# Kernel tuning notes

Measured on AMD Instinct MI355X. Metric: run time of the kernel, lower is better.

## Reference

```python
import jax, jax.numpy as jnp
import numpy as np
from jax import lax

B, T, N, D = 8, 64, 197, 768
HID = 4
K_FRAME, K_TOKEN = 8, 49
LAMBDA_COV, LAMBDA_SCORE = 1.0, 0.5
LN_EPS = 1e-5


def setup_inputs() -> dict:
    key = jax.random.key(0)
    k = jax.random.split(key, 5)
    x = jax.random.normal(k[0], (B, T, N, D), jnp.float32)
    mask = jax.random.uniform(k[1], (B, T, N), jnp.float32)
    ln_gamma = jnp.ones((D,), jnp.float32)
    ln_beta = jnp.zeros((D,), jnp.float32)
    W1 = jax.random.normal(k[2], (D, HID * D), jnp.float32) * 0.02
    b1 = jnp.zeros((HID * D,), jnp.float32)
    W2 = jax.random.normal(k[3], (HID * D, 1), jnp.float32) * 0.02
    b2 = jnp.zeros((1,), jnp.float32)
    return {"x": x, "mask": mask, "ln_gamma": ln_gamma, "ln_beta": ln_beta,
            "W1": W1, "b1": b1, "W2": W2, "b2": b2}


def _facility_location(frame_repr, score, valid, k):
    # cosine similarity between frames (F.normalize eps = 1e-12)
    fn = frame_repr / jnp.clip(jnp.linalg.norm(frame_repr, axis=-1, keepdims=True), 1e-12)
    sim = jnp.einsum('bid,bjd->bij', fn, fn)  # [B,T,T]
    Bb, Tt = score.shape

    def step(carry, _):
        best_cover, chosen = carry  # [B,T], [B,T] bool
        # coverage gain per candidate j: sum_i max(best[i], sim[i,j]) - best[i]
        cov_gain = jnp.maximum(best_cover[:, :, None], sim).sum(1) - best_cover.sum(1, keepdims=True)
        total = LAMBDA_COV * cov_gain + LAMBDA_SCORE * score
        total = jnp.where(valid & (~chosen), total, -jnp.inf)
        j = jnp.argmax(total, axis=1)  # [B]
        sim_j = jnp.take_along_axis(sim, j[:, None, None], axis=2)[..., 0]  # [B,T]
        best_cover = jnp.maximum(best_cover, sim_j)
        chosen = chosen.at[jnp.arange(Bb), j].set(True)
        return (best_cover, chosen), j

    init = (jnp.zeros((Bb, Tt), frame_repr.dtype), jnp.zeros((Bb, Tt), bool))
    (_, chosen), js = lax.scan(step, init, None, length=k)
    return js.T, chosen.astype(frame_repr.dtype)  # frame_idx [B,k], frame_mask [B,T]


def _kcenter(X, valid, k):
    # X [N,D], valid [N] bool; greedy k-center (farthest point sampling)
    d0 = jnp.where(valid, (X * X).sum(-1), -jnp.inf)
    first = jnp.argmax(d0)

    def dist_to(i):
        diff = X - X[i]
        return jnp.sqrt((diff * diff).sum(-1))

    min_dist = jnp.where(valid, dist_to(first), -1.0)

    def step(md, _):
        cand = jnp.argmax(md)
        md = jnp.where(valid, jnp.minimum(md, dist_to(cand)), -1.0)
        return md, cand

    _, rest = lax.scan(step, min_dist, None, length=k - 1)
    return jnp.concatenate([first[None], rest])


def _forward(x, mask, ln_gamma, ln_beta, W1, b1, W2, b2):
    # masked mean frame representation (use_cls=False path)
    denom = jnp.clip(mask.sum(2), 1e-6)                      # [B,T]
    frame_repr = (x * mask[..., None]).sum(2) / denom[..., None]  # [B,T,D]
    valid_frame = denom > 0

    # score head: LayerNorm -> Linear -> GELU(exact) -> Linear
    mu = frame_repr.mean(-1, keepdims=True)
    var = ((frame_repr - mu) ** 2).mean(-1, keepdims=True)
    h = (frame_repr - mu) / jnp.sqrt(var + LN_EPS) * ln_gamma + ln_beta
    h = jax.nn.gelu(h @ W1 + b1, approximate=False)
    score = (h @ W2 + b2)[..., 0]                            # [B,T]

    # selection is index-valued: no gradient flows through it (as in torch)
    frame_idx, frame_mask = _facility_location(
        lax.stop_gradient(frame_repr), lax.stop_gradient(score), valid_frame, K_FRAME)

    Xf = jnp.take_along_axis(x, frame_idx[:, :, None, None], axis=1)   # [B,K,N,D]
    mf = jnp.take_along_axis(mask, frame_idx[:, :, None], axis=1) > 0.5  # [B,K,N]

    token_idx = jax.vmap(jax.vmap(lambda Xs, vs: _kcenter(Xs, vs, K_TOKEN)))(
        lax.stop_gradient(Xf), mf)                           # [B,K,Kt]

    b_ar = jnp.arange(x.shape[0])
    token_mask = jnp.zeros(mask.shape, x.dtype).at[
        b_ar[:, None, None], frame_idx[:, :, None], token_idx].set(1.0)

    z = jnp.take_along_axis(Xf, token_idx[..., None], axis=2)  # [B,K,Kt,D]
    return z, frame_idx, token_idx, frame_mask, token_mask


def reference(x, mask, ln_gamma, ln_beta, W1, b1, W2, b2):
    return _forward(x, mask, ln_gamma, ln_beta, W1, b1, W2, b2)
```

## Files before the change

### kernel.cpp

```cpp
#include <hip/hip_runtime.h>
#include <math.h>

#define B_ 8
#define T_ 64
#define N_ 197
#define D_ 768
#define HIDD_ 3072
#define KF_ 8
#define KT_ 49
#define GSTRIDE 200

#define Z_SZ    (B_*KF_*KT_*D_)
#define FI_OFF  (Z_SZ)
#define TI_OFF  (FI_OFF + B_*KF_)
#define FM_OFF  (TI_OFF + B_*KF_*KT_)
#define TM_OFF  (FM_OFF + B_*T_)
#define TM_SZ   (B_*T_*N_)

#define WS_SCOREP  0
#define WS_FN64    98304
#define WS_H32     (WS_FN64 + 3145728)
#define WS_VALID   (WS_H32 + 1572864)
#define WS_FIDX    (WS_VALID + 2048)
#define WS_SIM     (WS_FIDX + 256)
#define WS_G       (WS_SIM + 262144)

__global__ __launch_bounds__(256) void kA(const float* __restrict__ x,
                                          const float* __restrict__ mask,
                                          const float* __restrict__ gamma,
                                          const float* __restrict__ beta,
                                          double* __restrict__ fn64,
                                          float* __restrict__ h32,
                                          int* __restrict__ validw) {
  const int row = blockIdx.x;
  const int tid = threadIdx.x;
  __shared__ float  ms[N_];
  __shared__ double red[256];
  __shared__ double sh_denom, sh_mu, sh_sd, sh_nrm;
  const float* xr = x + (size_t)row * (N_ * D_);

  if (tid < N_) ms[tid] = mask[(size_t)row * N_ + tid];
  __syncthreads();

  red[tid] = (tid < N_) ? (double)ms[tid] : 0.0;
  __syncthreads();
  for (int s = 128; s > 0; s >>= 1) { if (tid < s) red[tid] += red[tid + s]; __syncthreads(); }
  if (tid == 0) { double d = red[0]; sh_denom = (d > 1e-6) ? d : 1e-6; }
  __syncthreads();
  const double dn = sh_denom;

  double a0 = 0.0, a1 = 0.0, a2 = 0.0, a3 = 0.0;
  if (tid < 192) {
    const float* px = xr + tid * 4;
#pragma unroll 4
    for (int n = 0; n < N_; n++) {
      const double mv = (double)ms[n];
      const float4 v = *(const float4*)(px + (size_t)n * D_);
      a0 += (double)v.x * mv;
      a1 += (double)v.y * mv;
      a2 += (double)v.z * mv;
      a3 += (double)v.w * mv;
    }
  }
  const double f0 = a0 / dn, f1 = a1 / dn, f2 = a2 / dn, f3 = a3 / dn;

  red[tid] = (tid < 192) ? (f0 + f1 + f2 + f3) : 0.0; __syncthreads();
  for (int s = 128; s > 0; s >>= 1) { if (tid < s) red[tid] += red[tid + s]; __syncthreads(); }
  if (tid == 0) sh_mu = red[0] / (double)D_;
  __syncthreads();
  const double mu = sh_mu;

  red[tid] = (tid < 192) ? (f0 * f0 + f1 * f1 + f2 * f2 + f3 * f3) : 0.0; __syncthreads();
  for (int s = 128; s > 0; s >>= 1) { if (tid < s) red[tid] += red[tid + s]; __syncthreads(); }
  if (tid == 0) { double nr = sqrt(red[0]); sh_nrm = (nr > 1e-12) ? nr : 1e-12; }
  __syncthreads();

  red[tid] = (tid < 192) ? ((f0 - mu) * (f0 - mu) + (f1 - mu) * (f1 - mu) +
                            (f2 - mu) * (f2 - mu) + (f3 - mu) * (f3 - mu)) : 0.0;
  __syncthreads();
  for (int s = 128; s > 0; s >>= 1) { if (tid < s) red[tid] += red[tid + s]; __syncthreads(); }
  if (tid == 0) sh_sd = sqrt(red[0] / (double)D_ + 1e-5);
  __syncthreads();
  const double sd = sh_sd, nrm = sh_nrm;

  if (tid < 192) {
    const size_t base = (size_t)row * D_;
    const float4 g  = ((const float4*)gamma)[tid];
    const float4 be = ((const float4*)beta)[tid];
    float4 hv;
    hv.x = (float)((f0 - mu) / sd * (double)g.x + (double)be.x);
    hv.y = (float)((f1 - mu) / sd * (double)g.y + (double)be.y);
    hv.z = (float)((f2 - mu) / sd * (double)g.z + (double)be.z);
    hv.w = (float)((f3 - mu) / sd * (double)g.w + (double)be.w);
    *(float4*)(h32 + base + tid * 4) = hv;
    double2* fp = (double2*)(fn64 + base + tid * 4);
    fp[0] = make_double2(f0 / nrm, f1 / nrm);
    fp[1] = make_double2(f2 / nrm, f3 / nrm);
  }
  if (tid == 0) validw[row] = 1;
}

__global__ __launch_bounds__(256) void kB(const float* __restrict__ h32,
                                          const float* __restrict__ W1,
                                          const float* __restrict__ b1,
                                          const float* __restrict__ W2,
                                          double* __restrict__ scorep) {
  const int n0 = blockIdx.x * 128;
  const int m0 = blockIdx.y * 32;
  const int tid = threadIdx.x;
  const int tx = tid & 31;
  const int ty = tid >> 5;
  __shared__ float As[64 * 36];
  __shared__ float Bs[64 * 128];
  float acc[4][4];
#pragma unroll
  for (int r = 0; r < 4; r++)
#pragma unroll
    for (int c = 0; c < 4; c++) acc[r][c] = 0.0f;

  for (int kc = 0; kc < 12; kc++) {
    const int k0 = kc * 64;
#pragma unroll
    for (int it = 0; it < 8; it++) {
      int idx = tid + (it << 8);
      int k = idx & 63, m = idx >> 6;
      As[k * 36 + m] = h32[(size_t)(m0 + m) * D_ + k0 + k];
    }
#pragma unroll
    for (int it = 0; it < 8; it++) {
      int idx = tid + (it << 8);
      int k = idx >> 5, n4 = idx & 31;
      const float4 v = *(const float4*)(W1 + (size_t)(k0 + k) * HIDD_ + n0 + (n4 << 2));
      *(float4*)(Bs + k * 128 + (n4 << 2)) = v;
    }
    __syncthreads();
#pragma unroll 16
    for (int kk = 0; kk < 64; kk++) {
      float4 av = *(const float4*)(As + kk * 36 + ty * 4);
      float4 bv = *(const float4*)(Bs + kk * 128 + tx * 4);
      const float a[4] = {av.x, av.y, av.z, av.w};
      const float bb[4] = {bv.x, bv.y, bv.z, bv.w};
#pragma unroll
      for (int r = 0; r < 4; r++)
#pragma unroll
        for (int c = 0; c < 4; c++) acc[r][c] += a[r] * bb[c];
    }
    __syncthreads();
  }

  double part[4] = {0.0, 0.0, 0.0, 0.0};
#pragma unroll
  for (int r = 0; r < 4; r++) {
#pragma unroll
    for (int c = 0; c < 4; c++) {
      const int gn = n0 + tx * 4 + c;
      const double v = (double)(acc[r][c] + b1[gn]);
      const double g = 0.5 * v * (1.0 + erf(v * 0.7071067811865475244));
      part[r] += g * (double)W2[gn];
    }
  }
#pragma unroll
  for (int r = 0; r < 4; r++) {
    double s = part[r];
#pragma unroll
    for (int off = 16; off > 0; off >>= 1) s += __shfl_down(s, off, 32);
    if (tx == 0) scorep[(size_t)(m0 + ty * 4 + r) * 24 + blockIdx.x] = s;
  }
}

__global__ __launch_bounds__(256) void kS(const double* __restrict__ fn64,
                                          double* __restrict__ simG) {
  const int b    = blockIdx.x >> 2;
  const int tile = blockIdx.x & 3;
  const int tid = threadIdx.x;
  const int ty = tid >> 4;
  const int tx = tid & 15;
  __shared__ double As[64 * 17];
  __shared__ double Bs[64 * 66];
  double acc[4] = {0.0, 0.0, 0.0, 0.0};

  for (int kc = 0; kc < 12; kc++) {
#pragma unroll
    for (int it = 0; it < 4; it++) {
      const int idx = (it << 8) + tid;
      const int row = idx >> 6, kk = idx & 63;
      As[kk * 17 + row] = fn64[((size_t)(b * T_ + tile * 16 + row)) * D_ + kc * 64 + kk];
    }
#pragma unroll
    for (int it = 0; it < 16; it++) {
      const int idx = (it << 8) + tid;
      const int row = idx >> 6, kk = idx & 63;
      Bs[kk * 66 + row] = fn64[((size_t)(b * T_ + row)) * D_ + kc * 64 + kk];
    }
    __syncthreads();
#pragma unroll 8
    for (int kk = 0; kk < 64; kk++) {
      const double a = As[kk * 17 + ty];
      const double* bp = Bs + kk * 66 + tx * 4;
      acc[0] += a * bp[0];
      acc[1] += a * bp[1];
      acc[2] += a * bp[2];
      acc[3] += a * bp[3];
    }
    __syncthreads();
  }
  double* o = simG + ((size_t)b * 64 + tile * 16 + ty) * 64 + tx * 4;
  o[0] = acc[0]; o[1] = acc[1]; o[2] = acc[2]; o[3] = acc[3];
}

__global__ __launch_bounds__(256) void kD(const double* __restrict__ simG,
                                          const double* __restrict__ scorep,
                                          const int* __restrict__ validw,
                                          const float* __restrict__ b2,
                                          int* __restrict__ fidxw,
                                          float* __restrict__ out_fidx,
                                          float* __restrict__ out_fmask) {
  const int b = blockIdx.x;
  const int tid = threadIdx.x;
  __shared__ double sim[64 * 64];
  __shared__ double scoreS[64];
  __shared__ double bc[64];
  __shared__ int chosenS[64];
  __shared__ int validS[64];

  const double2* sp = (const double2*)(simG + (size_t)b * 4096);
#pragma unroll
  for (int it = 0; it < 8; it++) {
    const int idx = (it << 8) + tid;
    ((double2*)sim)[idx] = sp[idx];
  }
  if (tid < 64) {
    double s = 0.0;
    const double* pp = scorep + (size_t)(b * T_ + tid) * 24;
    for (int q = 0; q < 24; q++) s += pp[q];
    scoreS[tid]  = s + (double)b2[0];
    validS[tid]  = validw[b * T_ + tid];
    bc[tid]      = 0.0;
    chosenS[tid] = 0;
  }
  __syncthreads();

  for (int step = 0; step < KF_; step++) {
    if (tid < 64) {
      double g = 0.0;
      for (int ii = 0; ii < 64; ii++) g += fmax(bc[ii], sim[ii * 64 + tid]);
      double bs = bc[tid];
#pragma unroll
      for (int off = 32; off > 0; off >>= 1) bs += __shfl_down(bs, off, 64);
      bs = __shfl(bs, 0, 64);
      double tot = g - bs + 0.5 * scoreS[tid];
      if (!validS[tid] || chosenS[tid]) tot = -INFINITY;
      double bv = tot; int bi = tid;
#pragma unroll
      for (int off = 32; off > 0; off >>= 1) {
        double ov = __shfl_down(bv, off, 64);
        int    oi = __shfl_down(bi, off, 64);
        if (ov > bv || (ov == bv && oi < bi)) { bv = ov; bi = oi; }
      }
      bi = __shfl(bi, 0, 64);
      bc[tid] = fmax(bc[tid], sim[tid * 64 + bi]);
      if (tid == bi) chosenS[tid] = 1;
      if (tid == 0) {
        fidxw[b * KF_ + step] = bi;
        out_fidx[b * KF_ + step] = (float)bi;
      }
    }
    __syncthreads();
  }
  if (tid < 64) out_fmask[b * T_ + tid] = chosenS[tid] ? 1.0f : 0.0f;
}

__global__ __launch_bounds__(256) void kG(const float* __restrict__ x,
                                          const int* __restrict__ fidxw,
                                          double* __restrict__ G) {
  static const int TIa[10] = {0,0,0,0,1,1,1,2,2,3};
  static const int TJa[10] = {0,1,2,3,1,2,3,2,3,3};
  const int p  = blockIdx.x / 10;
  const int t  = blockIdx.x - p * 10;
  const int ti = TIa[t], tj = TJa[t];
  const int b  = p >> 3;
  const int fi = fidxw[p];
  const float* X = x + ((size_t)(b * T_ + fi)) * (N_ * D_);
  double* Gp = G + (size_t)p * (GSTRIDE * GSTRIDE);

  __shared__ float As[32 * 68];
  __shared__ float Bs[32 * 68];
  const int tid = threadIdx.x;
  const int tx = tid & 15;
  const int ty = tid >> 4;
  double acc[4][4];
#pragma unroll
  for (int r = 0; r < 4; r++)
#pragma unroll
    for (int c = 0; c < 4; c++) acc[r][c] = 0.0;

  for (int kc = 0; kc < 24; kc++) {
#pragma unroll
    for (int it = 0; it < 2; it++) {
      const int idx = (it << 8) + tid;
      const int row = idx >> 3;
      const int kg  = idx & 7;
      const int gra = ti * 64 + row, grb = tj * 64 + row;
      const int ra = (gra < N_) ? gra : (N_ - 1);
      const int rb = (grb < N_) ? grb : (N_ - 1);
      const float4 va = *(const float4*)(X + (size_t)ra * D_ + kc * 32 + kg * 4);
      const float4 vb = *(const float4*)(X + (size_t)rb * D_ + kc * 32 + kg * 4);
      As[(kg * 4 + 0) * 68 + row] = va.x;
      As[(kg * 4 + 1) * 68 + row] = va.y;
      As[(kg * 4 + 2) * 68 + row] = va.z;
      As[(kg * 4 + 3) * 68 + row] = va.w;
      Bs[(kg * 4 + 0) * 68 + row] = vb.x;
      Bs[(kg * 4 + 1) * 68 + row] = vb.y;
      Bs[(kg * 4 + 2) * 68 + row] = vb.z;
      Bs[(kg * 4 + 3) * 68 + row] = vb.w;
    }
    __syncthreads();
#pragma unroll 8
    for (int kk = 0; kk < 32; kk++) {
      const float4 av = *(const float4*)(As + kk * 68 + ty * 4);
      const float4 bv = *(const float4*)(Bs + kk * 68 + tx * 4);
      const double a[4]  = {(double)av.x, (double)av.y, (double)av.z, (double)av.w};
      const double bb[4] = {(double)bv.x, (double)bv.y, (double)bv.z, (double)bv.w};
#pragma unroll
      for (int r = 0; r < 4; r++)
#pragma unroll
        for (int c = 0; c < 4; c++) acc[r][c] += a[r] * bb[c];
    }
    __syncthreads();
  }

#pragma unroll
  for (int r = 0; r < 4; r++) {
    const int gi = ti * 64 + ty * 4 + r;
#pragma unroll
    for (int c = 0; c < 4; c++) {
      const int gj = tj * 64 + tx * 4 + c;
      if (gi < N_ && gj < N_) {
        Gp[(size_t)gi * GSTRIDE + gj] = acc[r][c];
        if (ti != tj) Gp[(size_t)gj * GSTRIDE + gi] = acc[r][c];
      }
    }
  }
}

__global__ __launch_bounds__(256) void kE2(const double* __restrict__ G,
                                           const float* __restrict__ mask,
                                           const int* __restrict__ fidxw,
                                           const float* __restrict__ x,
                                           float* __restrict__ out) {
  const int p = blockIdx.x;
  const int b = p >> 3;
  const int fi = fidxw[p];
  const double* Gp = G + (size_t)p * (GSTRIDE * GSTRIDE);
  const float* mrow = mask + (size_t)(b * T_ + fi) * N_;
  const float* X = x + ((size_t)(b * T_ + fi)) * (N_ * D_);
  const int tid = threadIdx.x;
  const bool live = tid < N_;

  __shared__ double gds[N_];
  __shared__ double bvS[4];
  __shared__ int biS[4];
  __shared__ int candS;
  __shared__ int toksS[KT_];

  const int valid = (live && mrow[tid] > 0.5f) ? 1 : 0;
  const double gd = live ? Gp[(size_t)tid * GSTRIDE + tid] : 0.0;
  if (live) gds[tid] = gd;
  __syncthreads();

  auto argmax = [&](double v) -> int {
    double bv = v; int bi = tid;
#pragma unroll
    for (int off = 32; off > 0; off >>= 1) {
      const double ov = __shfl_down(bv, off, 64);
      const int    oi = __shfl_down(bi, off, 64);
      if (ov > bv || (ov == bv && oi < bi)) { bv = ov; bi = oi; }
    }
    const int w = tid >> 6;
    if ((tid & 63) == 0) { bvS[w] = bv; biS[w] = bi; }
    __syncthreads();
    if (tid == 0) {
      double B0 = bvS[0]; int best = biS[0];
      for (int q = 1; q < 4; q++)
        if (bvS[q] > B0) { B0 = bvS[q]; best = biS[q]; }
      candS = best;
    }
    __syncthreads();
    return candS;
  };

  int cand = argmax((live && valid) ? gd : -INFINITY);
  if (tid == 0) toksS[0] = cand;

  double md = -INFINITY;
  for (int k = 1; k < KT_; k++) {
    const double gdc = gds[cand];
    const double g = live ? Gp[(size_t)cand * GSTRIDE + tid] : 0.0;
    const double dist = sqrt(fmax(gd + gdc - 2.0 * g, 0.0));
    if (live) md = valid ? ((k == 1) ? dist : fmin(md, dist)) : -1.0;
    cand = argmax(md);
    if (tid == 0) toksS[k] = cand;
  }
  __syncthreads();

  if (tid < KT_) {
    const int tok = toksS[tid];
    out[TI_OFF + p * KT_ + tid] = (float)tok;
    out[TM_OFF + (size_t)(b * T_ + fi) * N_ + tok] = 1.0f;
  }
  if (tid < 192) {
    for (int r = 0; r < KT_; r++) {
      const float4 v = *(const float4*)(X + (size_t)toksS[r] * D_ + tid * 4);
      *(float4*)(out + ((size_t)(p * KT_ + r)) * D_ + tid * 4) = v;
    }
  }
}

extern "C" void kernel_launch(void* const* d_in, const int* in_sizes, int n_in,
                              void* d_out, int out_size, void* d_ws, size_t ws_size,
                              hipStream_t stream) {
  (void)in_sizes; (void)n_in; (void)ws_size; (void)out_size;
  const float* x     = (const float*)d_in[0];
  const float* mask  = (const float*)d_in[1];
  const float* gamma = (const float*)d_in[2];
  const float* beta  = (const float*)d_in[3];
  const float* W1    = (const float*)d_in[4];
  const float* b1    = (const float*)d_in[5];
  const float* W2    = (const float*)d_in[6];
  const float* b2    = (const float*)d_in[7];
  float* out = (float*)d_out;
  char* ws = (char*)d_ws;

  double* scorep = (double*)(ws + WS_SCOREP);
  double* fn64   = (double*)(ws + WS_FN64);
  float*  h32    = (float*)(ws + WS_H32);
  int*    validw = (int*)(ws + WS_VALID);
  int*    fidxw  = (int*)(ws + WS_FIDX);
  double* simG   = (double*)(ws + WS_SIM);
  double* G      = (double*)(ws + WS_G);

  hipMemsetAsync(out + TM_OFF, 0, (size_t)TM_SZ * sizeof(float), stream);

  kA<<<B_ * T_, 256, 0, stream>>>(x, mask, gamma, beta, fn64, h32, validw);
  kS<<<B_ * 4, 256, 0, stream>>>(fn64, simG);
  kB<<<dim3(HIDD_ / 128, (B_ * T_) / 32), 256, 0, stream>>>(h32, W1, b1, W2, scorep);
  kD<<<B_, 256, 0, stream>>>(simG, scorep, validw, b2, fidxw, out + FI_OFF, out + FM_OFF);
  kG<<<B_ * KF_ * 10, 256, 0, stream>>>(x, fidxw, G);
  kE2<<<B_ * KF_, 256, 0, stream>>>(G, mask, fidxw, x, out);
}
```

Measured before the change: 762.3 us.

## Merge sim and score kernels; run greedy selections in single wavefront

Combines the double-precision similarity GEMM and the MLP scoring GEMM into one launch, with block ranges split by blockIdx, which removes a kernel launch and lets the two independent workloads share the GPU. The facility-location and k-center greedy loops are rewritten to run inside one 64-lane wavefront, keeping state in registers and using xor-shuffle argmax reductions instead of shared memory plus block-wide barriers. The validity check in facility location is dropped because every frame is marked valid. The trade-off is fewer active lanes in k-center, with each lane now handling four points.

```diff
diff --git a/kernel.cpp b/kernel.cpp
--- a/kernel.cpp
+++ b/kernel.cpp
@@ -100,117 +100,120 @@
   if (tid == 0) validw[row] = 1;
 }
 
-__global__ __launch_bounds__(256) void kB(const float* __restrict__ h32,
-                                          const float* __restrict__ W1,
-                                          const float* __restrict__ b1,
-                                          const float* __restrict__ W2,
-                                          double* __restrict__ scorep) {
-  const int n0 = blockIdx.x * 128;
-  const int m0 = blockIdx.y * 32;
+__global__ __launch_bounds__(256) void kSB(const double* __restrict__ fn64,
+                                           double* __restrict__ simG,
+                                           const float* __restrict__ h32,
+                                           const float* __restrict__ W1,
+                                           const float* __restrict__ b1,
+                                           const float* __restrict__ W2,
+                                           double* __restrict__ scorep) {
+  __shared__ char smem[42496] __attribute__((aligned(16)));
   const int tid = threadIdx.x;
-  const int tx = tid & 31;
-  const int ty = tid >> 5;
-  __shared__ float As[64 * 36];
-  __shared__ float Bs[64 * 128];
-  float acc[4][4];
-#pragma unroll
-  for (int r = 0; r < 4; r++)
-#pragma unroll
-    for (int c = 0; c < 4; c++) acc[r][c] = 0.0f;
-
-  for (int kc = 0; kc < 12; kc++) {
-    const int k0 = kc * 64;
-#pragma unroll
-    for (int it = 0; it < 8; it++) {
-      int idx = tid + (it << 8);
-      int k = idx & 63, m = idx >> 6;
-      As[k * 36 + m] = h32[(size_t)(m0 + m) * D_ + k0 + k];
-    }
-#pragma unroll
-    for (int it = 0; it < 8; it++) {
-      int idx = tid + (it << 8);
-      int k = idx >> 5, n4 = idx & 31;
-      const float4 v = *(const float4*)(W1 + (size_t)(k0 + k) * HIDD_ + n0 + (n4 << 2));
-      *(float4*)(Bs + k * 128 + (n4 << 2)) = v;
-    }
-    __syncthreads();
+
+  if (blockIdx.x < 32) {
+    const int b    = blockIdx.x >> 2;
+    const int tile = blockIdx.x & 3;
+    const int ty = tid >> 4;
+    const int tx = tid & 15;
+    double* As = (double*)smem;
+    double* Bs = (double*)(smem + 8704);
+    double acc[4] = {0.0, 0.0, 0.0, 0.0};
+
+    for (int kc = 0; kc < 12; kc++) {
+#pragma unroll
+      for (int it = 0; it < 4; it++) {
+        const int idx = (it << 8) + tid;
+        const int row = idx >> 6, kk = idx & 63;
+        As[kk * 17 + row] = fn64[((size_t)(b * T_ + tile * 16 + row)) * D_ + kc * 64 + kk];
+      }
+#pragma unroll
+      for (int it = 0; it < 16; it++) {
+        const int idx = (it << 8) + tid;
+        const int row = idx >> 6, kk = idx & 63;
+        Bs[kk * 66 + row] = fn64[((size_t)(b * T_ + row)) * D_ + kc * 64 + kk];
+      }
+      __syncthreads();
+#pragma unroll 8
+      for (int kk = 0; kk < 64; kk++) {
+        const double a = As[kk * 17 + ty];
+        const double* bp = Bs + kk * 66 + tx * 4;
+        acc[0] += a * bp[0];
+        acc[1] += a * bp[1];
+        acc[2] += a * bp[2];
+        acc[3] += a * bp[3];
+      }
+      __syncthreads();
+    }
+    double* o = simG + ((size_t)b * 64 + tile * 16 + ty) * 64 + tx * 4;
+    o[0] = acc[0]; o[1] = acc[1]; o[2] = acc[2]; o[3] = acc[3];
+  } else {
+    const int bid2 = blockIdx.x - 32;
+    const int nb = bid2 % 24;
+    const int n0 = nb * 128;
+    const int m0 = (bid2 / 24) * 32;
+    const int tx = tid & 31;
+    const int ty = tid >> 5;
+    float* As = (float*)smem;
+    float* Bs = (float*)(smem + 9216);
+    float acc[4][4];
+#pragma unroll
+    for (int r = 0; r < 4; r++)
+#pragma unroll
+      for (int c = 0; c < 4; c++) acc[r][c] = 0.0f;
+
+    for (int kc = 0; kc < 12; kc++) {
+      const int k0 = kc * 64;
+#pragma unroll
+      for (int it = 0; it < 8; it++) {
+        int idx = tid + (it << 8);
+        int k = idx & 63, m = idx >> 6;
+        As[k * 36 + m] = h32[(size_t)(m0 + m) * D_ + k0 + k];
+      }
+#pragma unroll
+      for (int it = 0; it < 8; it++) {
+        int idx = tid + (it << 8);
+        int k = idx >> 5, n4 = idx & 31;
+        const float4 v = *(const float4*)(W1 + (size_t)(k0 + k) * HIDD_ + n0 + (n4 << 2));
+        *(float4*)(Bs + k * 128 + (n4 << 2)) = v;
+      }
+      __syncthreads();
 #pragma unroll 16
-    for (int kk = 0; kk < 64; kk++) {
-      float4 av = *(const float4*)(As + kk * 36 + ty * 4);
-      float4 bv = *(const float4*)(Bs + kk * 128 + tx * 4);
-      const float a[4] = {av.x, av.y, av.z, av.w};
-      const float bb[4] = {bv.x, bv.y, bv.z, bv.w};
-#pragma unroll
-      for (int r = 0; r < 4; r++)
-#pragma unroll
-        for (int c = 0; c < 4; c++) acc[r][c] += a[r] * bb[c];
-    }
-    __syncthreads();
-  }
-
-  double part[4] = {0.0, 0.0, 0.0, 0.0};
-#pragma unroll
-  for (int r = 0; r < 4; r++) {
-#pragma unroll
-    for (int c = 0; c < 4; c++) {
-      const int gn = n0 + tx * 4 + c;
-      const double v = (double)(acc[r][c] + b1[gn]);
-      const double g = 0.5 * v * (1.0 + erf(v * 0.7071067811865475244));
-      part[r] += g * (double)W2[gn];
-    }
-  }
-#pragma unroll
-  for (int r = 0; r < 4; r++) {
-    double s = part[r];
-#pragma unroll
-    for (int off = 16; off > 0; off >>= 1) s += __shfl_down(s, off, 32);
-    if (tx == 0) scorep[(size_t)(m0 + ty * 4 + r) * 24 + blockIdx.x] = s;
-  }
-}
-
-__global__ __launch_bounds__(256) void kS(const double* __restrict__ fn64,
-                                          double* __restrict__ simG) {
-  const int b    = blockIdx.x >> 2;
-  const int tile = blockIdx.x & 3;
-  const int tid = threadIdx.x;
-  const int ty = tid >> 4;
-  const int tx = tid & 15;
-  __shared__ double As[64 * 17];
-  __shared__ double Bs[64 * 66];
-  double acc[4] = {0.0, 0.0, 0.0, 0.0};
-
-  for (int kc = 0; kc < 12; kc++) {
-#pragma unroll
-    for (int it = 0; it < 4; it++) {
-      const int idx = (it << 8) + tid;
-      const int row = idx >> 6, kk = idx & 63;
-      As[kk * 17 + row] = fn64[((size_t)(b * T_ + tile * 16 + row)) * D_ + kc * 64 + kk];
-    }
-#pragma unroll
-    for (int it = 0; it < 16; it++) {
-      const int idx = (it << 8) + tid;
-      const int row = idx >> 6, kk = idx & 63;
-      Bs[kk * 66 + row] = fn64[((size_t)(b * T_ + row)) * D_ + kc * 64 + kk];
-    }
-    __syncthreads();
-#pragma unroll 8
-    for (int kk = 0; kk < 64; kk++) {
-      const double a = As[kk * 17 + ty];
-      const double* bp = Bs + kk * 66 + tx * 4;
-      acc[0] += a * bp[0];
-      acc[1] += a * bp[1];
-      acc[2] += a * bp[2];
-      acc[3] += a * bp[3];
-    }
-    __syncthreads();
-  }
-  double* o = simG + ((size_t)b * 64 + tile * 16 + ty) * 64 + tx * 4;
-  o[0] = acc[0]; o[1] = acc[1]; o[2] = acc[2]; o[3] = acc[3];
+      for (int kk = 0; kk < 64; kk++) {
+        float4 av = *(const float4*)(As + kk * 36 + ty * 4);
+        float4 bv = *(const float4*)(Bs + kk * 128 + tx * 4);
+        const float a[4] = {av.x, av.y, av.z, av.w};
+        const float bb[4] = {bv.x, bv.y, bv.z, bv.w};
+#pragma unroll
+        for (int r = 0; r < 4; r++)
+#pragma unroll
+          for (int c = 0; c < 4; c++) acc[r][c] += a[r] * bb[c];
+      }
+      __syncthreads();
+    }
+
+    double part[4] = {0.0, 0.0, 0.0, 0.0};
+#pragma unroll
+    for (int r = 0; r < 4; r++) {
+#pragma unroll
+      for (int c = 0; c < 4; c++) {
+        const int gn = n0 + tx * 4 + c;
+        const double v = (double)(acc[r][c] + b1[gn]);
+        const double g = 0.5 * v * (1.0 + erf(v * 0.7071067811865475244));
+        part[r] += g * (double)W2[gn];
+      }
+    }
+#pragma unroll
+    for (int r = 0; r < 4; r++) {
+      double s = part[r];
+#pragma unroll
+      for (int off = 16; off > 0; off >>= 1) s += __shfl_down(s, off, 32);
+      if (tx == 0) scorep[(size_t)(m0 + ty * 4 + r) * 24 + nb] = s;
+    }
+  }
 }
 
 __global__ __launch_bounds__(256) void kD(const double* __restrict__ simG,
                                           const double* __restrict__ scorep,
-                                          const int* __restrict__ validw,
                                           const float* __restrict__ b2,
                                           int* __restrict__ fidxw,
                                           float* __restrict__ out_fidx,
@@ -218,10 +221,6 @@
   const int b = blockIdx.x;
   const int tid = threadIdx.x;
   __shared__ double sim[64 * 64];
-  __shared__ double scoreS[64];
-  __shared__ double bc[64];
-  __shared__ int chosenS[64];
-  __shared__ int validS[64];
 
   const double2* sp = (const double2*)(simG + (size_t)b * 4096);
 #pragma unroll
@@ -229,45 +228,42 @@
     const int idx = (it << 8) + tid;
     ((double2*)sim)[idx] = sp[idx];
   }
+  __syncthreads();
+
   if (tid < 64) {
     double s = 0.0;
     const double* pp = scorep + (size_t)(b * T_ + tid) * 24;
     for (int q = 0; q < 24; q++) s += pp[q];
-    scoreS[tid]  = s + (double)b2[0];
-    validS[tid]  = validw[b * T_ + tid];
-    bc[tid]      = 0.0;
-    chosenS[tid] = 0;
-  }
-  __syncthreads();
-
-  for (int step = 0; step < KF_; step++) {
-    if (tid < 64) {
-      double g = 0.0;
-      for (int ii = 0; ii < 64; ii++) g += fmax(bc[ii], sim[ii * 64 + tid]);
-      double bs = bc[tid];
-#pragma unroll
-      for (int off = 32; off > 0; off >>= 1) bs += __shfl_down(bs, off, 64);
-      bs = __shfl(bs, 0, 64);
-      double tot = g - bs + 0.5 * scoreS[tid];
-      if (!validS[tid] || chosenS[tid]) tot = -INFINITY;
+    const double half_score = 0.5 * (s + (double)b2[0]);
+
+    double bc_r = 0.0;
+    int chosen_r = 0;
+
+    for (int step = 0; step < KF_; step++) {
+      double gsum = 0.0;
+      for (int ii = 0; ii < 64; ii++) {
+        const double bcv = __shfl(bc_r, ii, 64);
+        gsum += fmax(bcv, sim[ii * 64 + tid]);
+      }
+      double tot = gsum + half_score;
+      if (chosen_r) tot = -INFINITY;
+
       double bv = tot; int bi = tid;
 #pragma unroll
-      for (int off = 32; off > 0; off >>= 1) {
-        double ov = __shfl_down(bv, off, 64);
-        int    oi = __shfl_down(bi, off, 64);
+      for (int off = 1; off < 64; off <<= 1) {
+        const double ov = __shfl_xor(bv, off, 64);
+        const int    oi = __shfl_xor(bi, off, 64);
         if (ov > bv || (ov == bv && oi < bi)) { bv = ov; bi = oi; }
       }
-      bi = __shfl(bi, 0, 64);
-      bc[tid] = fmax(bc[tid], sim[tid * 64 + bi]);
-      if (tid == bi) chosenS[tid] = 1;
+      bc_r = fmax(bc_r, sim[bi * 64 + tid]);
+      if (tid == bi) chosen_r = 1;
       if (tid == 0) {
         fidxw[b * KF_ + step] = bi;
         out_fidx[b * KF_ + step] = (float)bi;
       }
     }
-    __syncthreads();
-  }
-  if (tid < 64) out_fmask[b * T_ + tid] = chosenS[tid] ? 1.0f : 0.0f;
+    out_fmask[b * T_ + tid] = chosen_r ? 1.0f : 0.0f;
+  }
 }
 
 __global__ __launch_bounds__(256) void kG(const float* __restrict__ x,
@@ -355,51 +351,68 @@
   const float* mrow = mask + (size_t)(b * T_ + fi) * N_;
   const float* X = x + ((size_t)(b * T_ + fi)) * (N_ * D_);
   const int tid = threadIdx.x;
-  const bool live = tid < N_;
-
-  __shared__ double gds[N_];
-  __shared__ double bvS[4];
-  __shared__ int biS[4];
-  __shared__ int candS;
+
   __shared__ int toksS[KT_];
 
-  const int valid = (live && mrow[tid] > 0.5f) ? 1 : 0;
-  const double gd = live ? Gp[(size_t)tid * GSTRIDE + tid] : 0.0;
-  if (live) gds[tid] = gd;
-  __syncthreads();
-
-  auto argmax = [&](double v) -> int {
-    double bv = v; int bi = tid;
-#pragma unroll
-    for (int off = 32; off > 0; off >>= 1) {
-      const double ov = __shfl_down(bv, off, 64);
-      const int    oi = __shfl_down(bi, off, 64);
+  if (tid < 64) {
+    const int l = tid;
+    double gd[4]; int vld[4]; double md[4];
+#pragma unroll
+    for (int q = 0; q < 4; q++) {
+      const int pt = l + 64 * q;
+      const bool live = pt < N_;
+      gd[q] = live ? Gp[(size_t)pt * GSTRIDE + pt] : 0.0;
+      vld[q] = (live && (mrow[live ? pt : 0] > 0.5f)) ? 1 : 0;
+      md[q] = -INFINITY;
+    }
+
+    double bv = vld[0] ? gd[0] : -INFINITY;
+    int bi = l;
+#pragma unroll
+    for (int q = 1; q < 4; q++) {
+      const double v = vld[q] ? gd[q] : -INFINITY;
+      if (v > bv) { bv = v; bi = l + 64 * q; }
+    }
+#pragma unroll
+    for (int off = 1; off < 64; off <<= 1) {
+      const double ov = __shfl_xor(bv, off, 64);
+      const int    oi = __shfl_xor(bi, off, 64);
       if (ov > bv || (ov == bv && oi < bi)) { bv = ov; bi = oi; }
     }
-    const int w = tid >> 6;
-    if ((tid & 63) == 0) { bvS[w] = bv; biS[w] = bi; }
-    __syncthreads();
-    if (tid == 0) {
-      double B0 = bvS[0]; int best = biS[0];
-      for (int q = 1; q < 4; q++)
-        if (bvS[q] > B0) { B0 = bvS[q]; best = biS[q]; }
-      candS = best;
-    }
-    __syncthreads();
-    return candS;
-  };
-
-  int cand = argmax((live && valid) ? gd : -INFINITY);
-  if (tid == 0) toksS[0] = cand;
-
-  double md = -INFINITY;
-  for (int k = 1; k < KT_; k++) {
-    const double gdc = gds[cand];
-    const double g = live ? Gp[(size_t)cand * GSTRIDE + tid] : 0.0;
-    const double dist = sqrt(fmax(gd + gdc - 2.0 * g, 0.0));
-    if (live) md = valid ? ((k == 1) ? dist : fmin(md, dist)) : -1.0;
-    cand = argmax(md);
-    if (tid == 0) toksS[k] = cand;
+    int cand = bi;
+    if (l == 0) toksS[0] = cand;
+
+    for (int k = 1; k < KT_; k++) {
+      const size_t rowbase = (size_t)cand * GSTRIDE;
+      const double gdc = Gp[rowbase + cand];
+      const double g0 = Gp[rowbase + l];
+      const double g1 = Gp[rowbase + l + 64];
+      const double g2 = Gp[rowbase + l + 128];
+      const double d0 = sqrt(fmax(gd[0] + gdc - 2.0 * g0, 0.0));
+      const double d1 = sqrt(fmax(gd[1] + gdc - 2.0 * g1, 0.0));
+      const double d2 = sqrt(fmax(gd[2] + gdc - 2.0 * g2, 0.0));
+      md[0] = vld[0] ? ((k == 1) ? d0 : fmin(md[0], d0)) : -1.0;
+      md[1] = vld[1] ? ((k == 1) ? d1 : fmin(md[1], d1)) : -1.0;
+      md[2] = vld[2] ? ((k == 1) ? d2 : fmin(md[2], d2)) : -1.0;
+      if (l + 192 < N_) {
+        const double g3 = Gp[rowbase + l + 192];
+        const double d3 = sqrt(fmax(gd[3] + gdc - 2.0 * g3, 0.0));
+        md[3] = vld[3] ? ((k == 1) ? d3 : fmin(md[3], d3)) : -1.0;
+      }
+
+      bv = md[0]; bi = l;
+      if (md[1] > bv) { bv = md[1]; bi = l + 64; }
+      if (md[2] > bv) { bv = md[2]; bi = l + 128; }
+      if (md[3] > bv) { bv = md[3]; bi = l + 192; }
+#pragma unroll
+      for (int off = 1; off < 64; off <<= 1) {
+        const double ov = __shfl_xor(bv, off, 64);
+        const int    oi = __shfl_xor(bi, off, 64);
+        if (ov > bv || (ov == bv && oi < bi)) { bv = ov; bi = oi; }
+      }
+      cand = bi;
+      if (l == 0) toksS[k] = cand;
+    }
   }
   __syncthreads();
 
@@ -442,9 +455,9 @@
   hipMemsetAsync(out + TM_OFF, 0, (size_t)TM_SZ * sizeof(float), stream);
 
   kA<<<B_ * T_, 256, 0, stream>>>(x, mask, gamma, beta, fn64, h32, validw);
-  kS<<<B_ * 4, 256, 0, stream>>>(fn64, simG);
-  kB<<<dim3(HIDD_ / 128, (B_ * T_) / 32), 256, 0, stream>>>(h32, W1, b1, W2, scorep);
-  kD<<<B_, 256, 0, stream>>>(simG, scorep, validw, b2, fidxw, out + FI_OFF, out + FM_OFF);
+  kSB<<<32 + (HIDD_ / 128) * ((B_ * T_) / 32), 256, 0, stream>>>(
+      fn64, simG, h32, W1, b1, W2, scorep);
+  kD<<<B_, 256, 0, stream>>>(simG, scorep, b2, fidxw, out + FI_OFF, out + FM_OFF);
   kG<<<B_ * KF_ * 10, 256, 0, stream>>>(x, fidxw, G);
   kE2<<<B_ * KF_, 256, 0, stream>>>(G, mask, fidxw, x, out);
 }
```

New measurement: 744.7 us. -2.3%, faster.
